# Kernel tuning notes

Hardware: AMD Instinct MI355X
Metric: run time of the kernel (lower is better)

## Reference

```python
import jax, jax.numpy as jnp
import numpy as np

EPS = 1e-6


def setup_inputs() -> dict:
    key = jax.random.key(0)
    k = jax.random.split(key, 6)
    B, C_in, C_out, H, W, E = 32, 256, 256, 64, 64, 1024
    x = jax.random.normal(k[0], (B, C_in, H, W), dtype=jnp.float32)
    emb = jax.random.normal(k[1], (B, E), dtype=jnp.float32)
    # adaLN Linear(E -> 2*C_in). (Module zero-inits these; random here for coverage.)
    ada_w = jax.random.normal(k[2], (2 * C_in, E), dtype=jnp.float32) * 0.02
    ada_b = jax.random.normal(k[3], (2 * C_in,), dtype=jnp.float32) * 0.02
    # 1x1 Conv2d(C_in -> C_out) weight (C_out, C_in) and bias
    conv_w = jax.random.normal(k[4], (C_out, C_in), dtype=jnp.float32) * (1.0 / np.sqrt(C_in))
    conv_b = jax.random.normal(k[5], (C_out,), dtype=jnp.float32) * 0.02
    return {"x": x, "emb": emb, "ada_w": ada_w, "ada_b": ada_b,
            "conv_w": conv_w, "conv_b": conv_b}


def reference(x, emb, ada_w, ada_b, conv_w, conv_b):
    # adaLN modulation: SiLU(emb) @ W^T + b -> (B, 2C) -> shift, scale
    mod = jax.nn.silu(emb) @ ada_w.T + ada_b          # (B, 2C)
    shift, scale = jnp.split(mod, 2, axis=1)          # each (B, C)
    # RMSNorm over channel dim (no affine)
    rms = jax.lax.rsqrt(jnp.mean(x * x, axis=1, keepdims=True) + EPS)  # (B,1,H,W)
    xn = x * rms
    # modulate: x * (1 + scale) + shift, broadcast over H,W
    xm = xn * (1.0 + scale[:, :, None, None]) + shift[:, :, None, None]
    # 1x1 conv == channel GEMM
    y = jnp.einsum('bchw,oc->bohw', xm, conv_w) + conv_b[None, :, None, None]
    return jax.nn.selu(y)
```

## Files before the change

kernel.cpp:

```cpp
#include <hip/hip_runtime.h>
#include <hip/hip_bf16.h>

typedef __attribute__((ext_vector_type(4))) float f32x4;
typedef __attribute__((ext_vector_type(8))) short s16x8;
typedef __attribute__((ext_vector_type(4))) unsigned short u16x4;

__device__ __forceinline__ unsigned short f2bf(float f) {
  unsigned u = __builtin_bit_cast(unsigned, f);
  u += 0x7fffu + ((u >> 16) & 1u);
  return (unsigned short)(u >> 16);
}

__global__ __launch_bounds__(512) void k_mod(const float* __restrict__ emb,
                                             const float* __restrict__ ada_w,
                                             const float* __restrict__ ada_b,
                                             float* __restrict__ mod) {
  __shared__ __align__(16) float semb[32][1028];
  const int t = threadIdx.x;
  for (int i = t; i < 8192; i += 512) {
    f32x4 v = ((const f32x4*)emb)[i];
    f32x4 s;
#pragma unroll
    for (int j = 0; j < 4; ++j) s[j] = v[j] / (1.f + __expf(-v[j]));
    *(f32x4*)&semb[i >> 8][(i & 255) << 2] = s;
  }
  __syncthreads();
  const int jl = t >> 5, b = t & 31;
  const int j = blockIdx.x * 16 + jl;
  const f32x4* aw = (const f32x4*)(ada_w + (size_t)j * 1024);
  float acc = 0.f;
  for (int q = 0; q < 256; ++q) {
    f32x4 a = aw[q];
    f32x4 sv = *(const f32x4*)&semb[b][q * 4];
    acc += a[0] * sv[0] + a[1] * sv[1] + a[2] * sv[2] + a[3] * sv[3];
  }
  mod[b * 512 + j] = acc + ada_b[j];
}

__global__ __launch_bounds__(256) void k_prep(const float* __restrict__ mod,
                                              const float* __restrict__ conv_w,
                                              const float* __restrict__ conv_b,
                                              unsigned short* __restrict__ wp,
                                              float* __restrict__ dvec) {
  const int b = blockIdx.y;
  const int o = blockIdx.x * 4 + (threadIdx.x >> 6);
  const int l = threadIdx.x & 63;
  const float* sh = mod + b * 512;
  const float* sc = mod + b * 512 + 256;
  f32x4 cw = ((const f32x4*)(conv_w + (size_t)o * 256))[l];
  f32x4 s4 = ((const f32x4*)sc)[l];
  f32x4 h4 = ((const f32x4*)sh)[l];
  u16x4 wq;
#pragma unroll
  for (int j = 0; j < 4; ++j) wq[j] = f2bf(cw[j] * (1.f + s4[j]));
  const int wr = o >> 6, m = (o >> 4) & 3, lr = o & 15;
  const int kk = l >> 3, g = (l >> 1) & 3, jb = 4 * (l & 1);
  *(u16x4*)(wp + (size_t)b * 65536 + (((wr * 4 + m) * 8 + kk) * 512 + g * 128 + lr * 8 + jb)) = wq;
  float dd = cw[0] * h4[0] + cw[1] * h4[1] + cw[2] * h4[2] + cw[3] * h4[3];
#pragma unroll
  for (int off = 32; off; off >>= 1) dd += __shfl_down(dd, off);
  if (l == 0) dvec[b * 256 + o] = dd + conv_b[o];
}

__global__ __launch_bounds__(512, 2) void k_main(const float* __restrict__ x,
                                                 const unsigned short* __restrict__ wp,
                                                 const float* __restrict__ dvec,
                                                 float* __restrict__ out) {
  constexpr int HW = 4096;
  __shared__ __align__(16) unsigned char smem[81920];
  float(*xf)[32][256] = (float(*)[32][256])smem;
  unsigned char* bt = smem + 65536;
  float* prt = (float*)(smem + 65536);
  float* rms = (float*)(smem + 65536 + 1024);

  const int t = threadIdx.x;
  const int b = blockIdx.y;
  const int s0 = blockIdx.x * 256;
  const int w = t >> 6, lane = t & 63;
  const int wr = w >> 1, wc = w & 1;
  const int lr = lane & 15, g = lane >> 4;

  const float* xb = x + (size_t)b * (256 * HW) + s0;
  const unsigned short* A2 = wp + (size_t)b * 65536;

#define ISSUE(K, BUF)                                                                     \
  {                                                                                       \
    _Pragma("unroll") for (int i = 0; i < 4; ++i) {                                       \
      const float* gp = xb + (size_t)((K)*32 + w * 4 + i) * HW + lane * 4;                \
      void* lp = (void*)&xf[BUF][w * 4 + i][0];                                           \
      __builtin_amdgcn_global_load_lds((const __attribute__((address_space(1))) void*)gp, \
                                       (__attribute__((address_space(3))) void*)lp, 16,   \
                                       0, 0);                                             \
    }                                                                                     \
  }

  ISSUE(0, 0);
  ISSUE(1, 1);

  const int cg = lane >> 3;
  const int sl = 8 * w + (lane & 7);
  f32x4 ssq = {0.f, 0.f, 0.f, 0.f};

  f32x4 acc[4][8];
#pragma unroll
  for (int m = 0; m < 4; ++m)
#pragma unroll
    for (int n = 0; n < 8; ++n) acc[m][n] = f32x4{0.f, 0.f, 0.f, 0.f};

#pragma unroll
  for (int k = 0; k < 8; ++k) {
    const int buf = k & 1;
    if (k < 7) {
      asm volatile("s_waitcnt vmcnt(4)" ::: "memory");
    } else {
      asm volatile("s_waitcnt vmcnt(0)" ::: "memory");
    }
    asm volatile("s_waitcnt lgkmcnt(0)" ::: "memory");
    __builtin_amdgcn_s_barrier();

    f32x4 vv[4];
#pragma unroll
    for (int dc = 0; dc < 4; ++dc) vv[dc] = *(const f32x4*)&xf[buf][4 * cg + dc][4 * sl];
#pragma unroll
    for (int dc = 0; dc < 4; ++dc) ssq += vv[dc] * vv[dc];
#pragma unroll
    for (int si = 0; si < 4; ++si) {
      const int s = 4 * sl + si;
      const int vs = (s >> 4) & 3;
      u16x4 pk = {f2bf(vv[0][si]), f2bf(vv[1][si]), f2bf(vv[2][si]), f2bf(vv[3][si])};
      *(u16x4*)(bt + s * 64 + ((cg ^ (2 * vs)) << 3)) = pk;
    }
    asm volatile("s_waitcnt lgkmcnt(0)" ::: "memory");
    __builtin_amdgcn_s_barrier();

    s16x8 af[4];
#pragma unroll
    for (int m = 0; m < 4; ++m)
      af[m] = *(const s16x8*)(A2 + (((wr * 4 + m) * 8 + k) * 512 + lane * 8));
#pragma unroll
    for (int n = 0; n < 8; ++n) {
      const int s = 128 * wc + 16 * n + lr;
      const int vs = n & 3;
      s16x8 bf = *(const s16x8*)(bt + s * 64 + ((g ^ vs) << 4));
#pragma unroll
      for (int m = 0; m < 4; ++m)
        acc[m][n] = __builtin_amdgcn_mfma_f32_16x16x32_bf16(af[m], bf, acc[m][n], 0, 0, 0);
    }
    if (k < 6) ISSUE(k + 2, buf);
  }
#undef ISSUE

  asm volatile("s_waitcnt lgkmcnt(0)" ::: "memory");
  __syncthreads();
#pragma unroll
  for (int off = 8; off <= 32; off <<= 1) {
#pragma unroll
    for (int j = 0; j < 4; ++j) ssq[j] += __shfl_xor(ssq[j], off);
  }
  if (lane < 8) *(f32x4*)&prt[4 * (8 * w + lane)] = ssq;
  __syncthreads();
  if (t < 256) rms[t] = rsqrtf(prt[t] * (1.0f / 256.0f) + 1e-6f);
  __syncthreads();

  float rr[8];
#pragma unroll
  for (int n = 0; n < 8; ++n) rr[n] = rms[128 * wc + 16 * n + lr];
  float* ob = out + (size_t)b * (256 * HW) + s0;
#pragma unroll
  for (int m = 0; m < 4; ++m) {
    const int o0 = 64 * wr + 16 * m + 4 * g;
    const f32x4 dv = *(const f32x4*)(dvec + (size_t)b * 256 + o0);
#pragma unroll
    for (int n = 0; n < 8; ++n) {
#pragma unroll
      for (int r = 0; r < 4; ++r) {
        float v = rr[n] * acc[m][n][r] + dv[r];
        float res = v > 0.f ? 1.0507009873554805f * v
                            : 1.7580993408473766f * (__expf(v) - 1.f);
        ob[(size_t)(o0 + r) * HW + 128 * wc + 16 * n + lr] = res;
      }
    }
  }
}

extern "C" void kernel_launch(void* const* d_in, const int* in_sizes, int n_in,
                              void* d_out, int out_size, void* d_ws, size_t ws_size,
                              hipStream_t stream) {
  const float* x      = (const float*)d_in[0];
  const float* emb    = (const float*)d_in[1];
  const float* ada_w  = (const float*)d_in[2];
  const float* ada_b  = (const float*)d_in[3];
  const float* conv_w = (const float*)d_in[4];
  const float* conv_b = (const float*)d_in[5];
  float* out = (float*)d_out;

  float* mod  = (float*)d_ws;
  float* dvec = mod + 32 * 512;
  unsigned short* wp = (unsigned short*)(dvec + 32 * 256);

  k_mod<<<dim3(32), 512, 0, stream>>>(emb, ada_w, ada_b, mod);
  k_prep<<<dim3(64, 32), 256, 0, stream>>>(mod, conv_w, conv_b, wp, dvec);
  k_main<<<dim3(16, 32), 512, 0, stream>>>(x, wp, dvec, out);
}
```

Measured before the change: 98.85 us.

## Stage epilogue through LDS for coalesced stores; parallelize adaLN GEMV per batch

The main kernel's epilogue now writes activated results into an LDS tile, 64 output channels at a time, and each wave then streams full contiguous rows to global memory with 16-byte vector stores. Previously each lane issued scattered scalar stores of 16 floats per row. The modulation kernel now runs one block per (row-tile, batch) pair, each warp-segment splitting the dot product and reducing with shuffles, where before 32 blocks each did serial 1024-long loops. The LDS staging adds four barrier rounds plus extra LDS traffic. The k_mod grid grows to 1024 blocks, each recomputing SiLU for its own batch row.

After: 98.32 us. No clear change (-0.5%).

```diff
diff --git a/kernel.cpp b/kernel.cpp
--- a/kernel.cpp
+++ b/kernel.cpp
@@ -15,26 +15,31 @@
                                              const float* __restrict__ ada_w,
                                              const float* __restrict__ ada_b,
                                              float* __restrict__ mod) {
-  __shared__ __align__(16) float semb[32][1028];
+  __shared__ __align__(16) float se[1024];
   const int t = threadIdx.x;
-  for (int i = t; i < 8192; i += 512) {
-    f32x4 v = ((const f32x4*)emb)[i];
+  const int b = blockIdx.y;
+  if (t < 256) {
+    f32x4 v = ((const f32x4*)(emb + (size_t)b * 1024))[t];
     f32x4 s;
 #pragma unroll
     for (int j = 0; j < 4; ++j) s[j] = v[j] / (1.f + __expf(-v[j]));
-    *(f32x4*)&semb[i >> 8][(i & 255) << 2] = s;
-  }
-  __syncthreads();
-  const int jl = t >> 5, b = t & 31;
+    *(f32x4*)&se[4 * t] = s;
+  }
+  __syncthreads();
+  const int jl = t >> 5, l32 = t & 31;
   const int j = blockIdx.x * 16 + jl;
   const f32x4* aw = (const f32x4*)(ada_w + (size_t)j * 1024);
   float acc = 0.f;
-  for (int q = 0; q < 256; ++q) {
+#pragma unroll
+  for (int i = 0; i < 8; ++i) {
+    const int q = l32 + 32 * i;
     f32x4 a = aw[q];
-    f32x4 sv = *(const f32x4*)&semb[b][q * 4];
+    f32x4 sv = *(const f32x4*)&se[4 * q];
     acc += a[0] * sv[0] + a[1] * sv[1] + a[2] * sv[2] + a[3] * sv[3];
   }
-  mod[b * 512 + j] = acc + ada_b[j];
+#pragma unroll
+  for (int off = 1; off <= 16; off <<= 1) acc += __shfl_xor(acc, off);
+  if (l32 == 0) mod[b * 512 + j] = acc + ada_b[j];
 }
 
 __global__ __launch_bounds__(256) void k_prep(const float* __restrict__ mod,
@@ -70,8 +75,9 @@
   __shared__ __align__(16) unsigned char smem[81920];
   float(*xf)[32][256] = (float(*)[32][256])smem;
   unsigned char* bt = smem + 65536;
-  float* prt = (float*)(smem + 65536);
-  float* rms = (float*)(smem + 65536 + 1024);
+  float* epi = (float*)smem;
+  float* prt = (float*)(smem + 79872);
+  float* rms = (float*)(smem + 80896);
 
   const int t = threadIdx.x;
   const int b = blockIdx.y;
@@ -165,21 +171,38 @@
   float rr[8];
 #pragma unroll
   for (int n = 0; n < 8; ++n) rr[n] = rms[128 * wc + 16 * n + lr];
-  float* ob = out + (size_t)b * (256 * HW) + s0;
-#pragma unroll
-  for (int m = 0; m < 4; ++m) {
-    const int o0 = 64 * wr + 16 * m + 4 * g;
-    const f32x4 dv = *(const f32x4*)(dvec + (size_t)b * 256 + o0);
-#pragma unroll
-    for (int n = 0; n < 8; ++n) {
-#pragma unroll
-      for (int r = 0; r < 4; ++r) {
-        float v = rr[n] * acc[m][n][r] + dv[r];
-        float res = v > 0.f ? 1.0507009873554805f * v
-                            : 1.7580993408473766f * (__expf(v) - 1.f);
-        ob[(size_t)(o0 + r) * HW + 128 * wc + 16 * n + lr] = res;
+  const float* dvb = dvec + (size_t)b * 256;
+  float* obase = out + (size_t)b * (256 * HW) + s0;
+
+  for (int j = 0; j < 4; ++j) {
+    if (wr == j) {
+#pragma unroll
+      for (int m = 0; m < 4; ++m) {
+        const int ro = 16 * m + 4 * g;
+        const f32x4 dv = *(const f32x4*)(dvb + 64 * j + ro);
+#pragma unroll
+        for (int n = 0; n < 8; ++n) {
+          const int s = 128 * wc + 16 * n + lr;
+#pragma unroll
+          for (int r = 0; r < 4; ++r) {
+            float v = rr[n] * acc[m][n][r] + dv[r];
+            epi[(ro + r) * 260 + s] = v > 0.f ? 1.0507009873554805f * v
+                                              : 1.7580993408473766f * (__expf(v) - 1.f);
+          }
+        }
       }
     }
+    asm volatile("s_waitcnt lgkmcnt(0)" ::: "memory");
+    __builtin_amdgcn_s_barrier();
+    float* ob = obase + (size_t)(64 * j) * HW;
+#pragma unroll
+    for (int i = 0; i < 8; ++i) {
+      const int rl = w * 8 + i;
+      f32x4 vv = *(const f32x4*)&epi[rl * 260 + 4 * lane];
+      *(f32x4*)(ob + (size_t)rl * HW + 4 * lane) = vv;
+    }
+    asm volatile("s_waitcnt lgkmcnt(0)" ::: "memory");
+    __builtin_amdgcn_s_barrier();
   }
 }
 
@@ -198,7 +221,7 @@
   float* dvec = mod + 32 * 512;
   unsigned short* wp = (unsigned short*)(dvec + 32 * 256);
 
-  k_mod<<<dim3(32), 512, 0, stream>>>(emb, ada_w, ada_b, mod);
+  k_mod<<<dim3(32, 32), 512, 0, stream>>>(emb, ada_w, ada_b, mod);
   k_prep<<<dim3(64, 32), 256, 0, stream>>>(mod, conv_w, conv_b, wp, dvec);
   k_main<<<dim3(16, 32), 512, 0, stream>>>(x, wp, dvec, out);
 }
```
